# Optimization experiments

Measured on AMD Instinct MI355X. Metric: run time of the kernel, lower is better.

## Reference

```python
import math
import jax, jax.numpy as jnp
import numpy as np

B, S, E, H = 2, 2048, 1024, 16
D = E // H  # head_dim = 64
NEG = jnp.float32(-1e9)  # finite stand-in for masked_fill(-inf) to avoid NaN in attn @ V


def setup_inputs() -> dict:
    key = jax.random.key(0)
    ks = jax.random.split(key, 8)
    inp = {
        "query": jax.random.normal(ks[0], (B, S, E), jnp.float32),
        "key": jax.random.normal(ks[1], (B, S, E), jnp.float32),
        "value": jax.random.normal(ks[2], (B, S, E), jnp.float32),
        "Wq": jax.random.normal(ks[3], (E, E), jnp.float32) * 0.02,
        "bq": jnp.zeros((E,), jnp.float32),
        "Wk": jax.random.normal(ks[4], (E, E), jnp.float32) * 0.02,
        "bk": jnp.zeros((E,), jnp.float32),
        "Wv": jax.random.normal(ks[5], (E, E), jnp.float32) * 0.02,
        "bv": jnp.zeros((E,), jnp.float32),
        "pos_bias": jax.random.normal(ks[6], (H, 2 * S - 1), jnp.float32) * 0.02,
    }
    # gather indices: per-head row index [H,1,1] and relative-position index [S,S]
    inp["idx0"] = jnp.arange(H, dtype=jnp.int32).reshape(H, 1, 1)
    rel = np.arange(S)[:, None] - np.arange(S)[None, :] + (S - 1)  # in [0, 2S-2]
    inp["idx1"] = jnp.asarray(rel, jnp.int32)
    # causal boolean mask: True where masked (j > i)
    inp["mask"] = jnp.triu(jnp.ones((S, S), jnp.bool_), k=1)
    return inp


def _split(x):  # [B,S,E] -> [B,H,S,D]
    return x.reshape(B, S, H, D).transpose(0, 2, 1, 3)


def reference(query, key, value, Wq, bq, Wk, bk, Wv, bv, pos_bias, idx0, idx1, mask):
    q = _split(query @ Wq.T + bq)
    k = _split(key @ Wk.T + bk)
    v = _split(value @ Wv.T + bv)
    logits = jnp.einsum("bhqd,bhkd->bhqk", q, k) / math.sqrt(D)  # [B,H,S,S]
    logits = logits + pos_bias[idx0, idx1]  # gather -> [H,S,S], broadcast over B
    logits = jnp.where(mask, NEG, logits)   # masked_fill
    attn = jax.nn.log_softmax(logits, axis=-1)  # module uses LogSoftmax (faithful)
    out = jnp.einsum("bhqk,bhkd->bhqd", attn, v)
    return out.transpose(0, 2, 1, 3).reshape(B, S, E)
```

## Files before the change

kernel.cpp:

```cpp
#include <hip/hip_runtime.h>
#include <math.h>

constexpr int BB = 2;
constexpr int SS = 2048;
constexpr int EE = 1024;
constexpr int HH = 16;
constexpr int DD = 64;

typedef short short8 __attribute__((ext_vector_type(8)));
typedef short short4_t __attribute__((ext_vector_type(4)));
typedef float floatx4 __attribute__((ext_vector_type(4)));
typedef unsigned short ushort_t;

__device__ __forceinline__ ushort_t f2bf(float f) {
    unsigned int u = __float_as_uint(f);
    u += 0x7fffu + ((u >> 16) & 1u);
    return (ushort_t)(u >> 16);
}
__device__ __forceinline__ float bf2f(short s) {
    return __uint_as_float(((unsigned)(ushort_t)s) << 16);
}

__device__ __forceinline__ void gl_lds16(const void* g, void* l) {
    __builtin_amdgcn_global_load_lds(
        (const __attribute__((address_space(1))) void*)g,
        (__attribute__((address_space(3))) void*)l, 16, 0, 0);
}

__global__ __launch_bounds__(256) void repack_all(
    const float* __restrict__ x0, const float* __restrict__ x1, const float* __restrict__ x2,
    const float* __restrict__ w0, const float* __restrict__ w1, const float* __restrict__ w2,
    ushort_t* __restrict__ Xbf, ushort_t* __restrict__ Wbf)
{
    const int idx = blockIdx.x * 256 + threadIdx.x;
    const int row = idx >> 7;
    const int gir = idx & 127;
    const float* src;
    ushort_t* dst;
    int r;
    if (row < 3 * BB * SS) {
        const int z = row >> 12; r = row & (BB * SS - 1);
        src = (z == 0) ? x0 : (z == 1) ? x1 : x2;
        dst = Xbf + (size_t)z * BB * SS * EE;
    } else {
        const int rw = row - 3 * BB * SS;
        const int z = rw >> 10; r = rw & (EE - 1);
        src = (z == 0) ? w0 : (z == 1) ? w1 : w2;
        dst = Wbf + (size_t)z * EE * EE;
    }
    const int blk = gir >> 3, g = gir & 7;
    const int gp = g ^ (r & 7);
    const float* sp = src + (size_t)r * EE + gir * 8;
    float4 a = *(const float4*)sp;
    float4 b = *(const float4*)(sp + 4);
    short8 o;
    o[0] = (short)f2bf(a.x); o[1] = (short)f2bf(a.y); o[2] = (short)f2bf(a.z); o[3] = (short)f2bf(a.w);
    o[4] = (short)f2bf(b.x); o[5] = (short)f2bf(b.y); o[6] = (short)f2bf(b.z); o[7] = (short)f2bf(b.w);
    *(short8*)&dst[(size_t)r * EE + blk * 64 + gp * 8] = o;
}

__global__ __launch_bounds__(256) void proj_kernel(
    const ushort_t* __restrict__ Xall, const ushort_t* __restrict__ Wall,
    const float* __restrict__ bq, const float* __restrict__ bk, const float* __restrict__ bv,
    ushort_t* __restrict__ qb, ushort_t* __restrict__ kbb, ushort_t* __restrict__ vtb)
{
    __shared__ __align__(16) ushort_t Xs[128 * 64];
    __shared__ __align__(16) ushort_t Ws[128 * 64];

    const int z = blockIdx.z;
    const ushort_t* X = Xall + (size_t)z * BB * SS * EE;
    const ushort_t* W = Wall + (size_t)z * EE * EE;
    const float* bias = (z == 0) ? bq : (z == 1) ? bk : bv;

    const int t = threadIdx.x, w = t >> 6, l = t & 63, ln = t & 15, qd = (t >> 4) & 3;
    const int row0 = blockIdx.x * 128;
    const int col0 = blockIdx.y * 128;
    const int wzm = (w & 1) * 64, wzn = (w >> 1) * 64;

    floatx4 acc[4][4];
    #pragma unroll
    for (int i = 0; i < 4; ++i)
        #pragma unroll
        for (int j = 0; j < 4; ++j)
            acc[i][j] = (floatx4){0.f, 0.f, 0.f, 0.f};

    for (int k0 = 0; k0 < EE; k0 += 64) {
        __syncthreads();
        #pragma unroll
        for (int j = 0; j < 4; ++j) {
            const int c = w * 4 + j;
            const int r = c * 8 + (l >> 3);
            gl_lds16(&X[(size_t)(row0 + r) * EE + k0 + (l & 7) * 8], &Xs[c * 512]);
            gl_lds16(&W[(size_t)(col0 + r) * EE + k0 + (l & 7) * 8], &Ws[c * 512]);
        }
        __syncthreads();

        const ushort_t* Am = (z < 2) ? Ws : Xs;
        const ushort_t* Bn = (z < 2) ? Xs : Ws;
        #pragma unroll
        for (int kh = 0; kh < 2; ++kh) {
            const int sw = ((kh * 4 + qd) ^ (ln & 7)) * 8;
            short8 af[4], bfr[4];
            #pragma unroll
            for (int mi = 0; mi < 4; ++mi)
                af[mi] = *(const short8*)&Am[(wzm + mi * 16 + ln) * 64 + sw];
            #pragma unroll
            for (int ni = 0; ni < 4; ++ni)
                bfr[ni] = *(const short8*)&Bn[(wzn + ni * 16 + ln) * 64 + sw];
            #pragma unroll
            for (int mi = 0; mi < 4; ++mi)
                #pragma unroll
                for (int ni = 0; ni < 4; ++ni)
                    acc[mi][ni] = __builtin_amdgcn_mfma_f32_16x16x32_bf16(af[mi], bfr[ni], acc[mi][ni], 0, 0, 0);
        }
    }

    if (z < 2) {
        ushort_t* dst = z ? kbb : qb;
        #pragma unroll
        for (int mi = 0; mi < 4; ++mi) {
            const int o0 = col0 + wzm + mi * 16 + qd * 4;
            const float4 b4 = *(const float4*)&bias[o0];
            const int h = o0 >> 6, d0 = o0 & 63;
            const int g = d0 >> 3, dlow = d0 & 7;
            #pragma unroll
            for (int ni = 0; ni < 4; ++ni) {
                const int s = row0 + wzn + ni * 16 + ln;
                const int b = s >> 11, sr = s & (SS - 1);
                const int gp = g ^ (sr & 7);
                short4_t pk;
                pk[0] = (short)f2bf(acc[mi][ni][0] + b4.x);
                pk[1] = (short)f2bf(acc[mi][ni][1] + b4.y);
                pk[2] = (short)f2bf(acc[mi][ni][2] + b4.z);
                pk[3] = (short)f2bf(acc[mi][ni][3] + b4.w);
                *(short4_t*)&dst[((size_t)((b * HH + h) * SS) + sr) * DD + gp * 8 + dlow] = pk;
            }
        }
    } else {
        #pragma unroll
        for (int mi = 0; mi < 4; ++mi) {
            const int s0 = row0 + wzm + mi * 16 + qd * 4;
            const int b = s0 >> 11, sr0 = s0 & (SS - 1);
            const int sg = (sr0 >> 3) & 7, slow = sr0 & 7;
            #pragma unroll
            for (int ni = 0; ni < 4; ++ni) {
                const int o = col0 + wzn + ni * 16 + ln;
                const int h = o >> 6, d = o & 63;
                const float bvv = bias[o];
                const int gp2 = sg ^ (d & 7);
                short4_t pk;
                pk[0] = (short)f2bf(acc[mi][ni][0] + bvv);
                pk[1] = (short)f2bf(acc[mi][ni][1] + bvv);
                pk[2] = (short)f2bf(acc[mi][ni][2] + bvv);
                pk[3] = (short)f2bf(acc[mi][ni][3] + bvv);
                *(short4_t*)&vtb[((size_t)((b * HH + h) * DD) + d) * SS + (sr0 & ~63) + gp2 * 8 + slow] = pk;
            }
        }
    }
}

__global__ __launch_bounds__(256) void scan_chunks(
    const ushort_t* __restrict__ vtb, float* __restrict__ segs)
{
    const int t = threadIdx.x;
    const int d = blockIdx.x * 8 + (t >> 5);
    const int ch = t & 31;
    const int bh = blockIdx.y;
    const ushort_t* src = vtb + ((size_t)(bh * DD + d)) * SS + ch * 64;
    float s = 0.f;
    #pragma unroll
    for (int i = 0; i < 8; ++i) {
        short8 v = *(const short8*)&src[i * 8];
        #pragma unroll
        for (int j = 0; j < 8; ++j) s += bf2f(v[j]);
    }
    segs[((size_t)(bh * DD + d)) * 32 + ch] = s;
}

__global__ __launch_bounds__(256) void scan_finalize(
    const ushort_t* __restrict__ vtb, const float* __restrict__ segs,
    float* __restrict__ Sv, float* __restrict__ Tot)
{
    __shared__ float offp[4][64], subs[4][64];
    const int t = threadIdx.x, dd = t & 63, j = t >> 6;
    const int c = blockIdx.x, bh = blockIdx.y;

    float o = 0.f;
    for (int c2 = c + 1 + j; c2 < 32; c2 += 4)
        o += segs[((size_t)(bh * DD + dd)) * 32 + c2];
    offp[j][dd] = o;

    const ushort_t* vrow = vtb + ((size_t)(bh * DD + dd)) * SS + c * 64;
    const int g0 = (2 * j) ^ (dd & 7), g1 = (2 * j + 1) ^ (dd & 7);
    short8 a0 = *(const short8*)&vrow[g0 * 8];
    short8 a1 = *(const short8*)&vrow[g1 * 8];
    float arr[16];
    #pragma unroll
    for (int i = 0; i < 8; ++i) { arr[i] = bf2f(a0[i]); arr[8 + i] = bf2f(a1[i]); }
    float sub = 0.f;
    #pragma unroll
    for (int i = 0; i < 16; ++i) sub += arr[i];
    subs[j][dd] = sub;
    __syncthreads();

    float run = offp[0][dd] + offp[1][dd] + offp[2][dd] + offp[3][dd];
    for (int j2 = j + 1; j2 < 4; ++j2) run += subs[j2][dd];

    float* svp = Sv + ((size_t)bh * SS + c * 64 + j * 16) * DD + dd;
    for (int s = 15; s >= 0; --s) { svp[s * DD] = run; run += arr[s]; }
    if (c == 0 && j == 0) Tot[bh * DD + dd] = run;
}

__global__ __launch_bounds__(512, 4) void attn_kernel(
    const ushort_t* __restrict__ qb, const ushort_t* __restrict__ kbb,
    const ushort_t* __restrict__ vtb, const float* __restrict__ Sv,
    const float* __restrict__ Tot, const float* __restrict__ pb,
    float* __restrict__ out)
{
    __shared__ __align__(16) ushort_t Ks[2][64 * 64];
    __shared__ __align__(16) ushort_t Vt[2][64 * 64];
    __shared__ __align__(16) ushort_t Ls[128 * 76];
    __shared__ float pbL[2048];

    const int t = threadIdx.x, w = t >> 6, l = t & 63, ln = t & 15, qd = (t >> 4) & 3;
    const int id = blockIdx.x, bh = id & 31, tt = id >> 5;
    const int qt = (tt < 8) ? (15 - tt) : (tt - 8);
    const int b = bh >> 4, h = bh & 15, i0 = qt * 128;
    const int r0 = 16 * w;

    {
        const float* p = pb + h * (2 * SS - 1) + (SS - 1);
        *(float4*)&pbL[t * 4] = *(const float4*)&p[t * 4];
    }

    short8 qf[2];
    #pragma unroll
    for (int kh = 0; kh < 2; ++kh)
        qf[kh] = *(const short8*)&qb[((size_t)bh * SS + i0 + r0 + ln) * DD + (((kh * 4 + qd) ^ (ln & 7)) * 8)];

    floatx4 accpv[4];
    #pragma unroll
    for (int ct = 0; ct < 4; ++ct) accpv[ct] = (floatx4){0.f, 0.f, 0.f, 0.f};
    float part[4] = {};

    const int nkt = 2 * qt + 2;

    auto stage = [&](int buf, int kt) {
        const int k0 = kt * 64;
        const int row = w * 8 + (l >> 3), cg = l & 7;
        gl_lds16(&kbb[((size_t)bh * SS + k0 + row) * DD + cg * 8], &Ks[buf][w * 512]);
        gl_lds16(&vtb[((size_t)bh * DD + row) * SS + k0 + cg * 8], &Vt[buf][w * 512]);
    };

    stage(0, 0);
    for (int kt = 0; kt < nkt; ++kt) {
        __syncthreads();
        if (kt + 1 < nkt) stage((kt + 1) & 1, kt + 1);
        const ushort_t* KsC = Ks[kt & 1];
        const ushort_t* VtC = Vt[kt & 1];
        const int k0 = kt * 64, kdiag = i0 - k0;

        if (kdiag + r0 + 15 < 0) continue;

        floatx4 aq[4];
        #pragma unroll
        for (int ct = 0; ct < 4; ++ct) aq[ct] = (floatx4){0.f, 0.f, 0.f, 0.f};
        #pragma unroll
        for (int kh = 0; kh < 2; ++kh) {
            const int sw = ((kh * 4 + qd) ^ (ln & 7)) * 8;
            #pragma unroll
            for (int ct = 0; ct < 4; ++ct) {
                short8 bfr = *(const short8*)&KsC[(ct * 16 + ln) * 64 + sw];
                aq[ct] = __builtin_amdgcn_mfma_f32_16x16x32_bf16(qf[kh], bfr, aq[ct], 0, 0, 0);
            }
        }

        const int irel0 = r0 + qd * 4;
        unsigned* Ld = (unsigned*)Ls;
        const bool unmasked = (kt < 2 * qt);
        #pragma unroll
        for (int ct = 0; ct < 4; ++ct) {
            const int krel = ct * 16 + ln;
            const int pbase = kdiag + irel0 - krel;
            unsigned pk[4];
            #pragma unroll
            for (int reg = 0; reg < 4; ++reg) {
                unsigned u;
                if (unmasked) {
                    const float val = aq[ct][reg] * 0.125f + pbL[pbase + reg];
                    part[reg] += __expf(val);
                    u = __float_as_uint(val);
                } else {
                    const int rel = pbase + reg;
                    const bool ok = rel >= 0;
                    const float val = aq[ct][reg] * 0.125f + pbL[ok ? rel : 0];
                    part[reg] += ok ? __expf(val) : 0.f;
                    u = ok ? __float_as_uint(val) : 0u;
                }
                const unsigned nb = (unsigned)__builtin_amdgcn_mov_dpp((int)u, 0xF5, 0xF, 0xF, false);
                pk[reg] = __builtin_amdgcn_perm(nb, u, 0x07060302);
            }
            if (!(ln & 1)) {
                const int base = irel0 * 38 + (krel >> 1);
                Ld[base] = pk[0]; Ld[base + 38] = pk[1];
                Ld[base + 76] = pk[2]; Ld[base + 114] = pk[3];
            }
        }

        #pragma unroll
        for (int kh = 0; kh < 2; ++kh) {
            short8 af = *(const short8*)&Ls[(r0 + ln) * 76 + kh * 32 + qd * 8];
            const int sw = ((kh * 4 + qd) ^ (ln & 7)) * 8;
            #pragma unroll
            for (int ct = 0; ct < 4; ++ct) {
                short8 bfr = *(const short8*)&VtC[(ct * 16 + ln) * 64 + sw];
                accpv[ct] = __builtin_amdgcn_mfma_f32_16x16x32_bf16(af, bfr, accpv[ct], 0, 0, 0);
            }
        }
    }

    float lse[4];
    #pragma unroll
    for (int reg = 0; reg < 4; ++reg) {
        float p = part[reg];
        p += __shfl_xor(p, 1, 64);
        p += __shfl_xor(p, 2, 64);
        p += __shfl_xor(p, 4, 64);
        p += __shfl_xor(p, 8, 64);
        lse[reg] = __logf(p);
    }

    float tot[4];
    #pragma unroll
    for (int ct = 0; ct < 4; ++ct) tot[ct] = Tot[bh * DD + ct * 16 + ln];

    #pragma unroll
    for (int ct = 0; ct < 4; ++ct) {
        const int d = ct * 16 + ln;
        #pragma unroll
        for (int reg = 0; reg < 4; ++reg) {
            const int ig = i0 + r0 + qd * 4 + reg;
            const float sv = Sv[((size_t)bh * SS + ig) * DD + d];
            const float o = accpv[ct][reg] - lse[reg] * tot[ct] - 1e9f * sv;
            out[((size_t)(b * SS + ig)) * EE + h * DD + d] = o;
        }
    }
}

extern "C" void kernel_launch(void* const* d_in, const int* in_sizes, int n_in,
                              void* d_out, int out_size, void* d_ws, size_t ws_size,
                              hipStream_t stream)
{
    const float* query = (const float*)d_in[0];
    const float* key_  = (const float*)d_in[1];
    const float* value = (const float*)d_in[2];
    const float* Wq = (const float*)d_in[3];
    const float* bq = (const float*)d_in[4];
    const float* Wk = (const float*)d_in[5];
    const float* bk = (const float*)d_in[6];
    const float* Wv = (const float*)d_in[7];
    const float* bv = (const float*)d_in[8];
    const float* pb = (const float*)d_in[9];
    float* out = (float*)d_out;

    float* ws = (float*)d_ws;
    const size_t SZ = (size_t)BB * SS * EE;
    float* Svb  = ws;
    float* Totb = ws + SZ;
    float* segs = Totb + (size_t)BB * HH * DD;
    ushort_t* us  = (ushort_t*)(segs + (size_t)BB * HH * DD * 32);
    ushort_t* qbp = us;
    ushort_t* kbp = qbp + SZ;
    ushort_t* vtp = kbp + SZ;
    ushort_t* Xbf = vtp + SZ;
    ushort_t* Wbf = Xbf + 3 * SZ;

    const int ngroups = (3 * BB * SS + 3 * EE) * (EE / 8);
    repack_all<<<ngroups / 256, 256, 0, stream>>>(query, key_, value, Wq, Wk, Wv, Xbf, Wbf);

    proj_kernel<<<dim3(BB * SS / 128, EE / 128, 3), 256, 0, stream>>>(
        Xbf, Wbf, bq, bk, bv, qbp, kbp, vtp);

    scan_chunks<<<dim3(8, BB * HH), 256, 0, stream>>>(vtp, segs);
    scan_finalize<<<dim3(32, BB * HH), 256, 0, stream>>>(vtp, segs, Svb, Totb);

    attn_kernel<<<BB * HH * (SS / 128), 512, 0, stream>>>(
        qbp, kbp, vtp, Svb, Totb, pb, out);
}
```

Measured before the change: 260.2 us.

## Fuse masked-suffix V sums into attention and compute QK transposed to drop LDS staging

Removes the scan_finalize kernel and the full-size Sv suffix-sum buffer. The per-row masked-V suffix sums are now rebuilt inside the attention kernel from per-chunk segment sums loaded into LDS, plus an extra MFMA against a 0/1 upper-triangular mask fragment on the diagonal tile. The QK product is computed as K·Q so the probabilities land directly in the A-operand layout of 16x16x16 MFMAs, which removes the LDS round-trip (Ls buffer) and the DPP/perm packing. It also cuts the large fp32 Sv write and read. In exchange it adds extra MFMAs on the diagonal tiles and a 32-step segment reduction per thread in the epilogue.

```diff
diff --git a/kernel.cpp b/kernel.cpp
--- a/kernel.cpp
+++ b/kernel.cpp
@@ -174,55 +174,20 @@
         #pragma unroll
         for (int j = 0; j < 8; ++j) s += bf2f(v[j]);
     }
-    segs[((size_t)(bh * DD + d)) * 32 + ch] = s;
-}
-
-__global__ __launch_bounds__(256) void scan_finalize(
-    const ushort_t* __restrict__ vtb, const float* __restrict__ segs,
-    float* __restrict__ Sv, float* __restrict__ Tot)
-{
-    __shared__ float offp[4][64], subs[4][64];
-    const int t = threadIdx.x, dd = t & 63, j = t >> 6;
-    const int c = blockIdx.x, bh = blockIdx.y;
-
-    float o = 0.f;
-    for (int c2 = c + 1 + j; c2 < 32; c2 += 4)
-        o += segs[((size_t)(bh * DD + dd)) * 32 + c2];
-    offp[j][dd] = o;
-
-    const ushort_t* vrow = vtb + ((size_t)(bh * DD + dd)) * SS + c * 64;
-    const int g0 = (2 * j) ^ (dd & 7), g1 = (2 * j + 1) ^ (dd & 7);
-    short8 a0 = *(const short8*)&vrow[g0 * 8];
-    short8 a1 = *(const short8*)&vrow[g1 * 8];
-    float arr[16];
-    #pragma unroll
-    for (int i = 0; i < 8; ++i) { arr[i] = bf2f(a0[i]); arr[8 + i] = bf2f(a1[i]); }
-    float sub = 0.f;
-    #pragma unroll
-    for (int i = 0; i < 16; ++i) sub += arr[i];
-    subs[j][dd] = sub;
-    __syncthreads();
-
-    float run = offp[0][dd] + offp[1][dd] + offp[2][dd] + offp[3][dd];
-    for (int j2 = j + 1; j2 < 4; ++j2) run += subs[j2][dd];
-
-    float* svp = Sv + ((size_t)bh * SS + c * 64 + j * 16) * DD + dd;
-    for (int s = 15; s >= 0; --s) { svp[s * DD] = run; run += arr[s]; }
-    if (c == 0 && j == 0) Tot[bh * DD + dd] = run;
+    segs[((size_t)bh * 32 + ch) * 64 + d] = s;
 }
 
 __global__ __launch_bounds__(512, 4) void attn_kernel(
     const ushort_t* __restrict__ qb, const ushort_t* __restrict__ kbb,
-    const ushort_t* __restrict__ vtb, const float* __restrict__ Sv,
-    const float* __restrict__ Tot, const float* __restrict__ pb,
-    float* __restrict__ out)
+    const ushort_t* __restrict__ vtb, const float* __restrict__ segs,
+    const float* __restrict__ pb, float* __restrict__ out)
 {
     __shared__ __align__(16) ushort_t Ks[2][64 * 64];
     __shared__ __align__(16) ushort_t Vt[2][64 * 64];
-    __shared__ __align__(16) ushort_t Ls[128 * 76];
     __shared__ float pbL[2048];
-
-    const int t = threadIdx.x, w = t >> 6, l = t & 63, ln = t & 15, qd = (t >> 4) & 3;
+    __shared__ __align__(16) float segsL[32 * 64];
+
+    const int t = threadIdx.x, w = t >> 6, ln = t & 15, qd = (t >> 4) & 3;
     const int id = blockIdx.x, bh = id & 31, tt = id >> 5;
     const int qt = (tt < 8) ? (15 - tt) : (tt - 8);
     const int b = bh >> 4, h = bh & 15, i0 = qt * 128;
@@ -230,24 +195,31 @@
 
     {
         const float* p = pb + h * (2 * SS - 1) + (SS - 1);
-        *(float4*)&pbL[t * 4] = *(const float4*)&p[t * 4];
-    }
+        #pragma unroll
+        for (int j = 0; j < 4; ++j) pbL[t * 4 + j] = p[t * 4 + j];
+    }
+    gl_lds16(&segs[((size_t)bh * 32) * 64 + t * 4], &segsL[w * 256]);
 
     short8 qf[2];
     #pragma unroll
     for (int kh = 0; kh < 2; ++kh)
         qf[kh] = *(const short8*)&qb[((size_t)bh * SS + i0 + r0 + ln) * DD + (((kh * 4 + qd) ^ (ln & 7)) * 8)];
 
-    floatx4 accpv[4];
-    #pragma unroll
-    for (int ct = 0; ct < 4; ++ct) accpv[ct] = (floatx4){0.f, 0.f, 0.f, 0.f};
-    float part[4] = {};
+    floatx4 accpv[4], accsv[4];
+    #pragma unroll
+    for (int ct = 0; ct < 4; ++ct) {
+        accpv[ct] = (floatx4){0.f, 0.f, 0.f, 0.f};
+        accsv[ct] = (floatx4){0.f, 0.f, 0.f, 0.f};
+    }
+    float psum = 0.f;
 
     const int nkt = 2 * qt + 2;
+    const int ownkt = 2 * qt + (w >> 2);
+    const int iloc = (w & 3) * 16 + ln;
 
     auto stage = [&](int buf, int kt) {
         const int k0 = kt * 64;
-        const int row = w * 8 + (l >> 3), cg = l & 7;
+        const int row = t >> 3, cg = t & 7;
         gl_lds16(&kbb[((size_t)bh * SS + k0 + row) * DD + cg * 8], &Ks[buf][w * 512]);
         gl_lds16(&vtb[((size_t)bh * DD + row) * SS + k0 + cg * 8], &Vt[buf][w * 512]);
     };
@@ -256,83 +228,86 @@
     for (int kt = 0; kt < nkt; ++kt) {
         __syncthreads();
         if (kt + 1 < nkt) stage((kt + 1) & 1, kt + 1);
+        const int k0 = kt * 64, kdiag = i0 - k0;
+        if (kdiag + r0 + 15 < 0) continue;
         const ushort_t* KsC = Ks[kt & 1];
         const ushort_t* VtC = Vt[kt & 1];
-        const int k0 = kt * 64, kdiag = i0 - k0;
-
-        if (kdiag + r0 + 15 < 0) continue;
 
         floatx4 aq[4];
         #pragma unroll
-        for (int ct = 0; ct < 4; ++ct) aq[ct] = (floatx4){0.f, 0.f, 0.f, 0.f};
+        for (int mt = 0; mt < 4; ++mt) aq[mt] = (floatx4){0.f, 0.f, 0.f, 0.f};
         #pragma unroll
         for (int kh = 0; kh < 2; ++kh) {
             const int sw = ((kh * 4 + qd) ^ (ln & 7)) * 8;
             #pragma unroll
+            for (int mt = 0; mt < 4; ++mt) {
+                short8 af = *(const short8*)&KsC[(mt * 16 + ln) * 64 + sw];
+                aq[mt] = __builtin_amdgcn_mfma_f32_16x16x32_bf16(af, qf[kh], aq[mt], 0, 0, 0);
+            }
+        }
+
+        short4_t pfrag[4];
+        const bool full = (kdiag + r0 >= 63);
+        #pragma unroll
+        for (int mt = 0; mt < 4; ++mt) {
+            const int base = kdiag + r0 + ln - mt * 16 - qd * 4;
+            #pragma unroll
+            for (int reg = 0; reg < 4; ++reg) {
+                if (full) {
+                    const float val = aq[mt][reg] * 0.125f + pbL[base - reg];
+                    psum += __expf(val);
+                    pfrag[mt][reg] = (short)f2bf(val);
+                } else {
+                    const int rel = base - reg;
+                    const bool ok = rel >= 0;
+                    const float val = aq[mt][reg] * 0.125f + pbL[ok ? rel : 0];
+                    psum += ok ? __expf(val) : 0.f;
+                    pfrag[mt][reg] = ok ? (short)f2bf(val) : (short)0;
+                }
+            }
+        }
+
+        const bool own = (kt == ownkt);
+        #pragma unroll
+        for (int kk = 0; kk < 4; ++kk) {
+            short4_t uf;
+            if (own) {
+                #pragma unroll
+                for (int j = 0; j < 4; ++j)
+                    uf[j] = (kk * 16 + qd * 4 + j > iloc) ? (short)0x3F80 : (short)0;
+            }
+            #pragma unroll
             for (int ct = 0; ct < 4; ++ct) {
-                short8 bfr = *(const short8*)&KsC[(ct * 16 + ln) * 64 + sw];
-                aq[ct] = __builtin_amdgcn_mfma_f32_16x16x32_bf16(qf[kh], bfr, aq[ct], 0, 0, 0);
-            }
-        }
-
-        const int irel0 = r0 + qd * 4;
-        unsigned* Ld = (unsigned*)Ls;
-        const bool unmasked = (kt < 2 * qt);
-        #pragma unroll
-        for (int ct = 0; ct < 4; ++ct) {
-            const int krel = ct * 16 + ln;
-            const int pbase = kdiag + irel0 - krel;
-            unsigned pk[4];
-            #pragma unroll
-            for (int reg = 0; reg < 4; ++reg) {
-                unsigned u;
-                if (unmasked) {
-                    const float val = aq[ct][reg] * 0.125f + pbL[pbase + reg];
-                    part[reg] += __expf(val);
-                    u = __float_as_uint(val);
-                } else {
-                    const int rel = pbase + reg;
-                    const bool ok = rel >= 0;
-                    const float val = aq[ct][reg] * 0.125f + pbL[ok ? rel : 0];
-                    part[reg] += ok ? __expf(val) : 0.f;
-                    u = ok ? __float_as_uint(val) : 0u;
-                }
-                const unsigned nb = (unsigned)__builtin_amdgcn_mov_dpp((int)u, 0xF5, 0xF, 0xF, false);
-                pk[reg] = __builtin_amdgcn_perm(nb, u, 0x07060302);
-            }
-            if (!(ln & 1)) {
-                const int base = irel0 * 38 + (krel >> 1);
-                Ld[base] = pk[0]; Ld[base + 38] = pk[1];
-                Ld[base + 76] = pk[2]; Ld[base + 114] = pk[3];
-            }
-        }
-
-        #pragma unroll
-        for (int kh = 0; kh < 2; ++kh) {
-            short8 af = *(const short8*)&Ls[(r0 + ln) * 76 + kh * 32 + qd * 8];
-            const int sw = ((kh * 4 + qd) ^ (ln & 7)) * 8;
-            #pragma unroll
-            for (int ct = 0; ct < 4; ++ct) {
-                short8 bfr = *(const short8*)&VtC[(ct * 16 + ln) * 64 + sw];
-                accpv[ct] = __builtin_amdgcn_mfma_f32_16x16x32_bf16(af, bfr, accpv[ct], 0, 0, 0);
-            }
-        }
-    }
-
-    float lse[4];
-    #pragma unroll
-    for (int reg = 0; reg < 4; ++reg) {
-        float p = part[reg];
-        p += __shfl_xor(p, 1, 64);
-        p += __shfl_xor(p, 2, 64);
-        p += __shfl_xor(p, 4, 64);
-        p += __shfl_xor(p, 8, 64);
-        lse[reg] = __logf(p);
-    }
-
-    float tot[4];
-    #pragma unroll
-    for (int ct = 0; ct < 4; ++ct) tot[ct] = Tot[bh * DD + ct * 16 + ln];
+                const int off = (ct * 16 + ln) * 64 + (((kk * 2 + (qd >> 1)) ^ (ln & 7)) * 8 + (qd & 1) * 4);
+                short4_t bfr = *(const short4_t*)&VtC[off];
+                accpv[ct] = __builtin_amdgcn_mfma_f32_16x16x16bf16_1k(pfrag[kk], bfr, accpv[ct], 0, 0, 0);
+                if (own)
+                    accsv[ct] = __builtin_amdgcn_mfma_f32_16x16x16bf16_1k(uf, bfr, accsv[ct], 0, 0, 0);
+            }
+        }
+    }
+
+    float p = psum;
+    p += __shfl_xor(p, 16, 64);
+    p += __shfl_xor(p, 32, 64);
+    const float lseq = __logf(p);
+    float lseR[4];
+    #pragma unroll
+    for (int reg = 0; reg < 4; ++reg)
+        lseR[reg] = __shfl(lseq, qd * 4 + reg, 64);
+
+    const int cmin = 2 * qt + (w >> 2) + 1;
+    float tot[4], tail[4];
+    #pragma unroll
+    for (int ct = 0; ct < 4; ++ct) {
+        float T = 0.f, L = 0.f;
+        for (int c = 0; c < 32; ++c) {
+            const float s = segsL[c * 64 + ct * 16 + ln];
+            T += s;
+            if (c >= cmin) L += s;
+        }
+        tot[ct] = T; tail[ct] = L;
+    }
 
     #pragma unroll
     for (int ct = 0; ct < 4; ++ct) {
@@ -340,8 +315,8 @@
         #pragma unroll
         for (int reg = 0; reg < 4; ++reg) {
             const int ig = i0 + r0 + qd * 4 + reg;
-            const float sv = Sv[((size_t)bh * SS + ig) * DD + d];
-            const float o = accpv[ct][reg] - lse[reg] * tot[ct] - 1e9f * sv;
+            const float o = accpv[ct][reg] - lseR[reg] * tot[ct]
+                          - 1e9f * (accsv[ct][reg] + tail[ct]);
             out[((size_t)(b * SS + ig)) * EE + h * DD + d] = o;
         }
     }
@@ -365,10 +340,8 @@
 
     float* ws = (float*)d_ws;
     const size_t SZ = (size_t)BB * SS * EE;
-    float* Svb  = ws;
-    float* Totb = ws + SZ;
-    float* segs = Totb + (size_t)BB * HH * DD;
-    ushort_t* us  = (ushort_t*)(segs + (size_t)BB * HH * DD * 32);
+    float* segs = ws;
+    ushort_t* us  = (ushort_t*)(segs + (size_t)BB * HH * 32 * DD);
     ushort_t* qbp = us;
     ushort_t* kbp = qbp + SZ;
     ushort_t* vtp = kbp + SZ;
@@ -382,8 +355,7 @@
         Xbf, Wbf, bq, bk, bv, qbp, kbp, vtp);
 
     scan_chunks<<<dim3(8, BB * HH), 256, 0, stream>>>(vtp, segs);
-    scan_finalize<<<dim3(32, BB * HH), 256, 0, stream>>>(vtp, segs, Svb, Totb);
 
     attn_kernel<<<BB * HH * (SS / 128), 512, 0, stream>>>(
-        qbp, kbp, vtp, Svb, Totb, pb, out);
-}
+        qbp, kbp, vtp, segs, pb, out);
+}
```

Result: no change. 258.9 us (-0.5%).
